# Kernel tuning notes

Measured on AMD Instinct MI355X. Metric: run time of the kernel, lower is better.

Reference implementation:

```python
import jax, jax.numpy as jnp
import numpy as np

B, L, DIM = 2, 4096, 512
HEADS, KS = 8, 33
HEAD_DIM = DIM // HEADS
SCALE = HEAD_DIM ** -0.5


def setup_inputs() -> dict:
    key = jax.random.key(0)
    ks = jax.random.split(key, 5)
    s = 0.02
    return {
        "x": jax.random.normal(ks[0], (B, L, DIM), dtype=jnp.float32),
        "w_qkv": jax.random.normal(ks[1], (3 * DIM, DIM), dtype=jnp.float32) * s,
        "b_qkv": jax.random.normal(ks[2], (3 * DIM,), dtype=jnp.float32) * s,
        "w_proj": jax.random.normal(ks[3], (DIM, DIM), dtype=jnp.float32) * s,
        "b_proj": jax.random.normal(ks[4], (DIM,), dtype=jnp.float32) * s,
    }


def _na1d(q, k, v):
    # q,k,v: [B, L, H, d]. Each query i attends to KS tokens whose window
    # start is clamp(i - KS//2, 0, L-KS) (NATTEN boundary-clamped neighborhood).
    starts = jnp.clip(jnp.arange(L) - KS // 2, 0, L - KS)          # [L]
    idx = starts[:, None] + jnp.arange(KS)[None, :]                # [L, KS]
    k_g = k[:, idx]                                                # [B, L, KS, H, d]
    v_g = v[:, idx]                                                # [B, L, KS, H, d]
    scores = jnp.einsum("blhd,blkhd->bhlk", q * SCALE, k_g)        # [B, H, L, KS]
    attn = jax.nn.softmax(scores, axis=-1)
    out = jnp.einsum("bhlk,blkhd->blhd", attn, v_g)                # [B, L, H, d]
    return out


def reference(x, w_qkv, b_qkv, w_proj, b_proj):
    qkv = x @ w_qkv.T + b_qkv                                      # [B, L, 3*DIM]
    qkv = qkv.reshape(B, L, 3, HEADS, HEAD_DIM)
    q, k, v = qkv[:, :, 0], qkv[:, :, 1], qkv[:, :, 2]
    out = _na1d(q, k, v).reshape(B, L, DIM)
    return out @ w_proj.T + b_proj
```

## Files before the change

kernel.cpp:

```cpp
#include <hip/hip_runtime.h>
#include <hip/hip_bf16.h>

#define B_ 2
#define L_ 4096
#define DIM_ 512
#define HEADS_ 8
#define HDIM_ 64
#define KS_ 33
#define QKS_ 1024

typedef __bf16 bf16;
typedef __bf16 bf16x4 __attribute__((ext_vector_type(4)));
typedef __bf16 bf16x8 __attribute__((ext_vector_type(8)));
typedef float f32x4 __attribute__((ext_vector_type(4)));

typedef __attribute__((address_space(3))) void lds_void;
typedef __attribute__((address_space(1))) const void glb_void;

__device__ __forceinline__ void async_cp16(const bf16* g, bf16* l)
{
    __builtin_amdgcn_global_load_lds((glb_void*)g, (lds_void*)l, 16, 0, 0);
}

__global__ __launch_bounds__(256)
void cvt_all(const float* __restrict__ x,  const float* __restrict__ wq,
             const float* __restrict__ bq, const float* __restrict__ wp,
             const float* __restrict__ bp,
             bf16* __restrict__ xb,  bf16* __restrict__ wqb,
             bf16* __restrict__ bqb, bf16* __restrict__ wpb,
             bf16* __restrict__ bpb)
{
    const int blk = blockIdx.x;
    const float* src; bf16* dst; int n, base;
    if (blk < 2048)       { src = x;  dst = xb;  n = 4194304; base = blk; }
    else if (blk < 2432)  { src = wq; dst = wqb; n = 786432;  base = blk - 2048; }
    else if (blk < 2560)  { src = wp; dst = wpb; n = 262144;  base = blk - 2432; }
    else if (blk == 2560) { src = bq; dst = bqb; n = 1536;    base = 0; }
    else                  { src = bp; dst = bpb; n = 512;     base = 0; }
    int i = base * 2048 + threadIdx.x * 8;
    if (i + 8 <= n) {
        float4 a = *(const float4*)(src + i);
        float4 b = *(const float4*)(src + i + 4);
        bf16x8 o;
        o[0] = (bf16)a.x; o[1] = (bf16)a.y; o[2] = (bf16)a.z; o[3] = (bf16)a.w;
        o[4] = (bf16)b.x; o[5] = (bf16)b.y; o[6] = (bf16)b.z; o[7] = (bf16)b.w;
        *(bf16x8*)(dst + i) = o;
    }
}

__global__ __launch_bounds__(256)
void gemm_qkv(const bf16* __restrict__ A, const bf16* __restrict__ W,
              const bf16* __restrict__ bias,
              bf16* __restrict__ qk, bf16* __restrict__ vT)
{
    __shared__ bf16 As[128][64];
    __shared__ bf16 Bs[64][64];

    const int tid  = threadIdx.x;
    const int wave = tid >> 6;
    const int lane = tid & 63;
    const int wm   = (wave >> 1) * 64;
    const int wn   = (wave & 1) * 32;
    const int l16  = lane & 15;
    const int quad = lane >> 4;

    const int row0 = blockIdx.x * 128;
    const int col0 = blockIdx.y * 64;
    const int K    = DIM_;

    f32x4 acc[4][2] = {};

    for (int k0 = 0; k0 < K; k0 += 64) {
        #pragma unroll
        for (int it = 0; it < 6; ++it) {
            int f = it * 256 + tid;
            if (f < 1024) {
                int r = f >> 3, pc = f & 7, lc = pc ^ (r & 7);
                async_cp16(&A[(size_t)(row0 + r) * K + k0 + lc * 8], &As[r][pc * 8]);
            } else {
                int g = f - 1024;
                int r = g >> 3, pc = g & 7, lc = pc ^ (r & 7);
                async_cp16(&W[(size_t)(col0 + r) * K + k0 + lc * 8], &Bs[r][pc * 8]);
            }
        }
        __syncthreads();

        #pragma unroll
        for (int ks = 0; ks < 2; ++ks) {
            bf16x8 af[4], bfr[2];
            #pragma unroll
            for (int i = 0; i < 4; ++i) {
                int ra = wm + i * 16 + l16;
                af[i] = *(const bf16x8*)(&As[ra][((ks * 4 + quad) ^ (ra & 7)) * 8]);
            }
            #pragma unroll
            for (int i = 0; i < 2; ++i) {
                int rb = wn + i * 16 + l16;
                bfr[i] = *(const bf16x8*)(&Bs[rb][((ks * 4 + quad) ^ (rb & 7)) * 8]);
            }
            #pragma unroll
            for (int mi = 0; mi < 4; ++mi)
                #pragma unroll
                for (int ni = 0; ni < 2; ++ni)
                    acc[mi][ni] = __builtin_amdgcn_mfma_f32_16x16x32_bf16(
                        af[mi], bfr[ni], acc[mi][ni], 0, 0, 0);
        }
        __syncthreads();
    }

    if (col0 < 1024) {
        #pragma unroll
        for (int ni = 0; ni < 2; ++ni) {
            int n = col0 + wn + ni * 16 + l16;
            float bv = (float)bias[n];
            #pragma unroll
            for (int mi = 0; mi < 4; ++mi) {
                int mrow = row0 + wm + mi * 16 + quad * 4;
                #pragma unroll
                for (int r = 0; r < 4; ++r)
                    qk[(size_t)(mrow + r) * QKS_ + n] = (bf16)(acc[mi][ni][r] + bv);
            }
        }
    } else {
        #pragma unroll
        for (int ni = 0; ni < 2; ++ni) {
            int nf = col0 + wn + ni * 16 + l16;
            float bv = (float)bias[nf];
            int hd = nf - 1024;
            #pragma unroll
            for (int mi = 0; mi < 4; ++mi) {
                int m = row0 + wm + mi * 16 + quad * 4;
                int b = m >> 12;
                int l = m & (L_ - 1);
                bf16x4 v4;
                #pragma unroll
                for (int r = 0; r < 4; ++r) v4[r] = (bf16)(acc[mi][ni][r] + bv);
                *(bf16x4*)(vT + ((size_t)(b * DIM_ + hd)) * L_ + l) = v4;
            }
        }
    }
}

__global__ __launch_bounds__(256)
void gemm_proj(const bf16* __restrict__ A, const bf16* __restrict__ W,
               const bf16* __restrict__ bias, float* __restrict__ C)
{
    __shared__ bf16 As[64][64];
    __shared__ bf16 Bs[64][64];

    const int tid  = threadIdx.x;
    const int wave = tid >> 6;
    const int lane = tid & 63;
    const int wm   = (wave & 1) * 32;
    const int wn   = (wave >> 1) * 32;
    const int l16  = lane & 15;
    const int quad = lane >> 4;

    const int row0 = blockIdx.x * 64;
    const int col0 = blockIdx.y * 64;
    const int K    = DIM_;

    f32x4 acc[2][2] = {};

    for (int k0 = 0; k0 < K; k0 += 64) {
        #pragma unroll
        for (int it = 0; it < 4; ++it) {
            int f = it * 256 + tid;
            if (f < 512) {
                int r = f >> 3, pc = f & 7, lc = pc ^ (r & 7);
                async_cp16(&A[(size_t)(row0 + r) * K + k0 + lc * 8], &As[r][pc * 8]);
            } else {
                int g = f - 512;
                int r = g >> 3, pc = g & 7, lc = pc ^ (r & 7);
                async_cp16(&W[(size_t)(col0 + r) * K + k0 + lc * 8], &Bs[r][pc * 8]);
            }
        }
        __syncthreads();

        #pragma unroll
        for (int ks = 0; ks < 2; ++ks) {
            bf16x8 af[2], bfr[2];
            #pragma unroll
            for (int i = 0; i < 2; ++i) {
                int ra = wm + i * 16 + l16;
                af[i] = *(const bf16x8*)(&As[ra][((ks * 4 + quad) ^ (ra & 7)) * 8]);
            }
            #pragma unroll
            for (int i = 0; i < 2; ++i) {
                int rb = wn + i * 16 + l16;
                bfr[i] = *(const bf16x8*)(&Bs[rb][((ks * 4 + quad) ^ (rb & 7)) * 8]);
            }
            #pragma unroll
            for (int mi = 0; mi < 2; ++mi)
                #pragma unroll
                for (int ni = 0; ni < 2; ++ni)
                    acc[mi][ni] = __builtin_amdgcn_mfma_f32_16x16x32_bf16(
                        af[mi], bfr[ni], acc[mi][ni], 0, 0, 0);
        }
        __syncthreads();
    }

    #pragma unroll
    for (int ni = 0; ni < 2; ++ni) {
        int n = col0 + wn + ni * 16 + l16;
        float bv = (float)bias[n];
        #pragma unroll
        for (int mi = 0; mi < 2; ++mi) {
            int mrow = row0 + wm + mi * 16 + quad * 4;
            #pragma unroll
            for (int r = 0; r < 4; ++r)
                C[(size_t)(mrow + r) * DIM_ + n] = acc[mi][ni][r] + bv;
        }
    }
}

__global__ __launch_bounds__(128)
void na1d_attn_mfma(const bf16* __restrict__ qk, const bf16* __restrict__ vT,
                    bf16* __restrict__ att)
{
    __shared__ bf16 Klds[64 * 64];
    __shared__ bf16 Plds[2][16][72];

    const int tid  = threadIdx.x;
    const int wave = tid >> 6;
    const int lane = tid & 63;
    const int l16  = lane & 15;
    const int quad = lane >> 4;

    const int xcd  = blockIdx.x & 7;
    const int s    = blockIdx.x >> 3;
    const int qtr  = s & 3;
    const int jj   = (s >> 2) & 3;
    const int h    = (s >> 4) & 7;
    const int b    = s >> 7;
    const int p    = jj * 8 + xcd;
    const int Q0   = p * 128 + qtr * 32;

    const size_t rowbase = (size_t)b * L_;

    #pragma unroll
    for (int i = 0; i < 4; ++i) {
        int ck = i * 128 + tid;
        int r  = ck >> 3;
        int pc = ck & 7;
        int lc = pc ^ (r & 7);
        int g  = Q0 - 16 + r;
        g = g < 0 ? 0 : (g > L_ - 1 ? L_ - 1 : g);
        async_cp16(qk + (rowbase + g) * QKS_ + DIM_ + h * HDIM_ + lc * 8,
                   Klds + (size_t)ck * 8);
    }

    const int q0w = Q0 + wave * 16;
    const bf16* qptr = qk + (rowbase + q0w + l16) * QKS_ + h * HDIM_ + quad * 8;
    bf16x8 qf0 = *(const bf16x8*)(qptr);
    bf16x8 qf1 = *(const bf16x8*)(qptr + 32);

    int k_base = q0w - 16;
    if (k_base > L_ - 48) k_base = L_ - 48;
    if (k_base < 0) k_base = 0;
    const int rel = k_base - (Q0 - 16);

    __syncthreads();

    f32x4 sacc[3] = {};
    #pragma unroll
    for (int t = 0; t < 3; ++t) {
        int r = rel + t * 16 + l16;
        bf16x8 kf0 = *(const bf16x8*)(Klds + r * 64 + ((quad ^ (r & 7)) * 8));
        bf16x8 kf1 = *(const bf16x8*)(Klds + r * 64 + (((4 + quad) ^ (r & 7)) * 8));
        sacc[t] = __builtin_amdgcn_mfma_f32_16x16x32_bf16(qf0, kf0, sacc[t], 0, 0, 0);
        sacc[t] = __builtin_amdgcn_mfma_f32_16x16x32_bf16(qf1, kf1, sacc[t], 0, 0, 0);
    }

    int offr[4];
    #pragma unroll
    for (int r = 0; r < 4; ++r) {
        int lq = q0w + quad * 4 + r;
        int st = lq - KS_ / 2;
        if (st < 0) st = 0;
        if (st > L_ - KS_) st = L_ - KS_;
        offr[r] = st - k_base;
    }
    float sv[3][4];
    #pragma unroll
    for (int t = 0; t < 3; ++t) {
        int j = t * 16 + l16;
        #pragma unroll
        for (int r = 0; r < 4; ++r) {
            float xv = sacc[t][r] * 0.125f;
            sv[t][r] = (j >= offr[r] && j <= offr[r] + 32) ? xv : -1e30f;
        }
    }

    float mr[4], sum[4];
    #pragma unroll
    for (int r = 0; r < 4; ++r)
        mr[r] = fmaxf(fmaxf(sv[0][r], sv[1][r]), sv[2][r]);
    #pragma unroll
    for (int o = 1; o < 16; o <<= 1)
        #pragma unroll
        for (int r = 0; r < 4; ++r)
            mr[r] = fmaxf(mr[r], __shfl_xor(mr[r], o, 64));
    #pragma unroll
    for (int t = 0; t < 3; ++t)
        #pragma unroll
        for (int r = 0; r < 4; ++r)
            sv[t][r] = __expf(sv[t][r] - mr[r]);
    #pragma unroll
    for (int r = 0; r < 4; ++r)
        sum[r] = sv[0][r] + sv[1][r] + sv[2][r];
    #pragma unroll
    for (int o = 1; o < 16; o <<= 1)
        #pragma unroll
        for (int r = 0; r < 4; ++r)
            sum[r] += __shfl_xor(sum[r], o, 64);
    #pragma unroll
    for (int r = 0; r < 4; ++r) {
        float inv = 1.0f / sum[r];
        #pragma unroll
        for (int t = 0; t < 3; ++t) sv[t][r] *= inv;
    }

    bf16* P = &Plds[wave][0][0];
    {
        int rr = lane >> 2;
        int c0 = 48 + (lane & 3) * 4;
        *(bf16x4*)(&P[rr * 72 + c0]) = (bf16x4){(bf16)0.f, (bf16)0.f, (bf16)0.f, (bf16)0.f};
    }
    #pragma unroll
    for (int t = 0; t < 3; ++t)
        #pragma unroll
        for (int r = 0; r < 4; ++r)
            P[(quad * 4 + r) * 72 + t * 16 + l16] = (bf16)sv[t][r];
    __syncthreads();

    bf16x8 pf0 = *(const bf16x8*)(&P[l16 * 72 + quad * 8]);
    bf16x8 pf1 = *(const bf16x8*)(&P[l16 * 72 + 32 + quad * 8]);

    const bf16* vbase = vT + (size_t)(b * DIM_ + h * HDIM_) * L_;
    int c1 = k_base + quad * 8;
    int c2 = k_base + 32 + quad * 8;
    if (c2 > L_ - 8) c2 = L_ - 8;
    f32x4 o[4] = {};
    #pragma unroll
    for (int t = 0; t < 4; ++t) {
        const bf16* vrow = vbase + (size_t)(t * 16 + l16) * L_;
        bf16x8 vf0 = *(const bf16x8*)(vrow + c1);
        bf16x8 vf1 = *(const bf16x8*)(vrow + c2);
        o[t] = __builtin_amdgcn_mfma_f32_16x16x32_bf16(pf0, vf0, o[t], 0, 0, 0);
        o[t] = __builtin_amdgcn_mfma_f32_16x16x32_bf16(pf1, vf1, o[t], 0, 0, 0);
    }

    bf16* orow = att + (rowbase + q0w) * DIM_ + h * HDIM_;
    #pragma unroll
    for (int t = 0; t < 4; ++t)
        #pragma unroll
        for (int r = 0; r < 4; ++r)
            orow[(size_t)(quad * 4 + r) * DIM_ + t * 16 + l16] = (bf16)o[t][r];
}

extern "C" void kernel_launch(void* const* d_in, const int* in_sizes, int n_in,
                              void* d_out, int out_size, void* d_ws, size_t ws_size,
                              hipStream_t stream) {
    const int n_x  = B_ * L_ * DIM_;
    const int n_wq = 3 * DIM_ * DIM_;
    const int n_bq = 3 * DIM_;
    const int n_wp = DIM_ * DIM_;
    const int n_bp = DIM_;

    char* ws = (char*)d_ws;
    bf16* xb  = (bf16*)ws;
    bf16* wqb = xb  + n_x;
    bf16* bqb = wqb + n_wq;
    bf16* wpb = bqb + n_bq;
    bf16* bpb = wpb + n_wp;
    bf16* qk  = bpb + n_bp;
    bf16* vT  = qk  + (size_t)8192 * 1024;
    bf16* att = vT  + (size_t)B_ * DIM_ * L_;

    float* out = (float*)d_out;
    const int M = B_ * L_;

    cvt_all<<<2562, 256, 0, stream>>>(
        (const float*)d_in[0], (const float*)d_in[1], (const float*)d_in[2],
        (const float*)d_in[3], (const float*)d_in[4],
        xb, wqb, bqb, wpb, bpb);

    gemm_qkv<<<dim3(M / 128, (3 * DIM_) / 64), 256, 0, stream>>>(
        xb, wqb, bqb, qk, vT);

    na1d_attn_mfma<<<dim3((B_ * HEADS_ * L_) / 32), 128, 0, stream>>>(qk, vT, att);

    gemm_proj<<<dim3(M / 64, DIM_ / 64), 256, 0, stream>>>(
        att, wpb, bpb, out);
}
```

Before: 118.5 us.

## Fuse x fp32-to-bf16 conversion into QKV GEMM, enlarge attention and proj tiles

Drops the separate conversion pass over x and instead converts fp32 x to bf16 while staging it into LDS inside the QKV GEMM, which removes a full write and reread of the bf16 copy of x. The attention kernel now handles 64 queries with 4 waves per block, sharing a 96-row K tile. The projection GEMM reuses the 128-row tile shape. The trade-off is that the x loads in the QKV GEMM become synchronous register loads instead of async LDS copies, and x is reloaded and reconverted for each of the 24 column blocks.

```diff
diff --git a/kernel.cpp b/kernel.cpp
--- a/kernel.cpp
+++ b/kernel.cpp
@@ -23,20 +23,17 @@
 }
 
 __global__ __launch_bounds__(256)
-void cvt_all(const float* __restrict__ x,  const float* __restrict__ wq,
-             const float* __restrict__ bq, const float* __restrict__ wp,
-             const float* __restrict__ bp,
-             bf16* __restrict__ xb,  bf16* __restrict__ wqb,
-             bf16* __restrict__ bqb, bf16* __restrict__ wpb,
-             bf16* __restrict__ bpb)
+void cvt_w(const float* __restrict__ wq, const float* __restrict__ bq,
+           const float* __restrict__ wp, const float* __restrict__ bp,
+           bf16* __restrict__ wqb, bf16* __restrict__ bqb,
+           bf16* __restrict__ wpb, bf16* __restrict__ bpb)
 {
     const int blk = blockIdx.x;
     const float* src; bf16* dst; int n, base;
-    if (blk < 2048)       { src = x;  dst = xb;  n = 4194304; base = blk; }
-    else if (blk < 2432)  { src = wq; dst = wqb; n = 786432;  base = blk - 2048; }
-    else if (blk < 2560)  { src = wp; dst = wpb; n = 262144;  base = blk - 2432; }
-    else if (blk == 2560) { src = bq; dst = bqb; n = 1536;    base = 0; }
-    else                  { src = bp; dst = bpb; n = 512;     base = 0; }
+    if (blk < 384)        { src = wq; dst = wqb; n = 786432; base = blk; }
+    else if (blk < 512)   { src = wp; dst = wpb; n = 262144; base = blk - 384; }
+    else if (blk == 512)  { src = bq; dst = bqb; n = 1536;   base = 0; }
+    else                  { src = bp; dst = bpb; n = 512;    base = 0; }
     int i = base * 2048 + threadIdx.x * 8;
     if (i + 8 <= n) {
         float4 a = *(const float4*)(src + i);
@@ -49,9 +46,107 @@
 }
 
 __global__ __launch_bounds__(256)
-void gemm_qkv(const bf16* __restrict__ A, const bf16* __restrict__ W,
+void gemm_qkv(const float* __restrict__ X, const bf16* __restrict__ W,
               const bf16* __restrict__ bias,
               bf16* __restrict__ qk, bf16* __restrict__ vT)
+{
+    __shared__ bf16 As[128][64];
+    __shared__ bf16 Bs[64][64];
+
+    const int tid  = threadIdx.x;
+    const int wave = tid >> 6;
+    const int lane = tid & 63;
+    const int wm   = (wave >> 1) * 64;
+    const int wn   = (wave & 1) * 32;
+    const int l16  = lane & 15;
+    const int quad = lane >> 4;
+
+    const int row0 = blockIdx.x * 128;
+    const int col0 = blockIdx.y * 64;
+    const int K    = DIM_;
+
+    f32x4 acc[4][2] = {};
+
+    for (int k0 = 0; k0 < K; k0 += 64) {
+        #pragma unroll
+        for (int it = 0; it < 2; ++it) {
+            int g = it * 256 + tid;
+            int r = g >> 3, pc = g & 7, lc = pc ^ (r & 7);
+            async_cp16(&W[(size_t)(col0 + r) * K + k0 + lc * 8], &Bs[r][pc * 8]);
+        }
+        #pragma unroll
+        for (int it = 0; it < 4; ++it) {
+            int f = it * 256 + tid;
+            int r = f >> 3, pc = f & 7, lc = pc ^ (r & 7);
+            const float* src = X + (size_t)(row0 + r) * K + k0 + lc * 8;
+            float4 a = *(const float4*)src;
+            float4 b = *(const float4*)(src + 4);
+            bf16x8 o;
+            o[0] = (bf16)a.x; o[1] = (bf16)a.y; o[2] = (bf16)a.z; o[3] = (bf16)a.w;
+            o[4] = (bf16)b.x; o[5] = (bf16)b.y; o[6] = (bf16)b.z; o[7] = (bf16)b.w;
+            *(bf16x8*)(&As[r][pc * 8]) = o;
+        }
+        __syncthreads();
+
+        #pragma unroll
+        for (int ks = 0; ks < 2; ++ks) {
+            bf16x8 af[4], bfr[2];
+            #pragma unroll
+            for (int i = 0; i < 4; ++i) {
+                int ra = wm + i * 16 + l16;
+                af[i] = *(const bf16x8*)(&As[ra][((ks * 4 + quad) ^ (ra & 7)) * 8]);
+            }
+            #pragma unroll
+            for (int i = 0; i < 2; ++i) {
+                int rb = wn + i * 16 + l16;
+                bfr[i] = *(const bf16x8*)(&Bs[rb][((ks * 4 + quad) ^ (rb & 7)) * 8]);
+            }
+            #pragma unroll
+            for (int mi = 0; mi < 4; ++mi)
+                #pragma unroll
+                for (int ni = 0; ni < 2; ++ni)
+                    acc[mi][ni] = __builtin_amdgcn_mfma_f32_16x16x32_bf16(
+                        af[mi], bfr[ni], acc[mi][ni], 0, 0, 0);
+        }
+        __syncthreads();
+    }
+
+    if (col0 < 1024) {
+        #pragma unroll
+        for (int ni = 0; ni < 2; ++ni) {
+            int n = col0 + wn + ni * 16 + l16;
+            float bv = (float)bias[n];
+            #pragma unroll
+            for (int mi = 0; mi < 4; ++mi) {
+                int mrow = row0 + wm + mi * 16 + quad * 4;
+                #pragma unroll
+                for (int r = 0; r < 4; ++r)
+                    qk[(size_t)(mrow + r) * QKS_ + n] = (bf16)(acc[mi][ni][r] + bv);
+            }
+        }
+    } else {
+        #pragma unroll
+        for (int ni = 0; ni < 2; ++ni) {
+            int nf = col0 + wn + ni * 16 + l16;
+            float bv = (float)bias[nf];
+            int hd = nf - 1024;
+            #pragma unroll
+            for (int mi = 0; mi < 4; ++mi) {
+                int m = row0 + wm + mi * 16 + quad * 4;
+                int b = m >> 12;
+                int l = m & (L_ - 1);
+                bf16x4 v4;
+                #pragma unroll
+                for (int r = 0; r < 4; ++r) v4[r] = (bf16)(acc[mi][ni][r] + bv);
+                *(bf16x4*)(vT + ((size_t)(b * DIM_ + hd)) * L_ + l) = v4;
+            }
+        }
+    }
+}
+
+__global__ __launch_bounds__(256)
+void gemm_proj(const bf16* __restrict__ A, const bf16* __restrict__ W,
+               const bf16* __restrict__ bias, float* __restrict__ C)
 {
     __shared__ bf16 As[128][64];
     __shared__ bf16 Bs[64][64];
@@ -108,104 +203,12 @@
         __syncthreads();
     }
 
-    if (col0 < 1024) {
-        #pragma unroll
-        for (int ni = 0; ni < 2; ++ni) {
-            int n = col0 + wn + ni * 16 + l16;
-            float bv = (float)bias[n];
-            #pragma unroll
-            for (int mi = 0; mi < 4; ++mi) {
-                int mrow = row0 + wm + mi * 16 + quad * 4;
-                #pragma unroll
-                for (int r = 0; r < 4; ++r)
-                    qk[(size_t)(mrow + r) * QKS_ + n] = (bf16)(acc[mi][ni][r] + bv);
-            }
-        }
-    } else {
-        #pragma unroll
-        for (int ni = 0; ni < 2; ++ni) {
-            int nf = col0 + wn + ni * 16 + l16;
-            float bv = (float)bias[nf];
-            int hd = nf - 1024;
-            #pragma unroll
-            for (int mi = 0; mi < 4; ++mi) {
-                int m = row0 + wm + mi * 16 + quad * 4;
-                int b = m >> 12;
-                int l = m & (L_ - 1);
-                bf16x4 v4;
-                #pragma unroll
-                for (int r = 0; r < 4; ++r) v4[r] = (bf16)(acc[mi][ni][r] + bv);
-                *(bf16x4*)(vT + ((size_t)(b * DIM_ + hd)) * L_ + l) = v4;
-            }
-        }
-    }
-}
-
-__global__ __launch_bounds__(256)
-void gemm_proj(const bf16* __restrict__ A, const bf16* __restrict__ W,
-               const bf16* __restrict__ bias, float* __restrict__ C)
-{
-    __shared__ bf16 As[64][64];
-    __shared__ bf16 Bs[64][64];
-
-    const int tid  = threadIdx.x;
-    const int wave = tid >> 6;
-    const int lane = tid & 63;
-    const int wm   = (wave & 1) * 32;
-    const int wn   = (wave >> 1) * 32;
-    const int l16  = lane & 15;
-    const int quad = lane >> 4;
-
-    const int row0 = blockIdx.x * 64;
-    const int col0 = blockIdx.y * 64;
-    const int K    = DIM_;
-
-    f32x4 acc[2][2] = {};
-
-    for (int k0 = 0; k0 < K; k0 += 64) {
-        #pragma unroll
-        for (int it = 0; it < 4; ++it) {
-            int f = it * 256 + tid;
-            if (f < 512) {
-                int r = f >> 3, pc = f & 7, lc = pc ^ (r & 7);
-                async_cp16(&A[(size_t)(row0 + r) * K + k0 + lc * 8], &As[r][pc * 8]);
-            } else {
-                int g = f - 512;
-                int r = g >> 3, pc = g & 7, lc = pc ^ (r & 7);
-                async_cp16(&W[(size_t)(col0 + r) * K + k0 + lc * 8], &Bs[r][pc * 8]);
-            }
-        }
-        __syncthreads();
-
-        #pragma unroll
-        for (int ks = 0; ks < 2; ++ks) {
-            bf16x8 af[2], bfr[2];
-            #pragma unroll
-            for (int i = 0; i < 2; ++i) {
-                int ra = wm + i * 16 + l16;
-                af[i] = *(const bf16x8*)(&As[ra][((ks * 4 + quad) ^ (ra & 7)) * 8]);
-            }
-            #pragma unroll
-            for (int i = 0; i < 2; ++i) {
-                int rb = wn + i * 16 + l16;
-                bfr[i] = *(const bf16x8*)(&Bs[rb][((ks * 4 + quad) ^ (rb & 7)) * 8]);
-            }
-            #pragma unroll
-            for (int mi = 0; mi < 2; ++mi)
-                #pragma unroll
-                for (int ni = 0; ni < 2; ++ni)
-                    acc[mi][ni] = __builtin_amdgcn_mfma_f32_16x16x32_bf16(
-                        af[mi], bfr[ni], acc[mi][ni], 0, 0, 0);
-        }
-        __syncthreads();
-    }
-
     #pragma unroll
     for (int ni = 0; ni < 2; ++ni) {
         int n = col0 + wn + ni * 16 + l16;
         float bv = (float)bias[n];
         #pragma unroll
-        for (int mi = 0; mi < 2; ++mi) {
+        for (int mi = 0; mi < 4; ++mi) {
             int mrow = row0 + wm + mi * 16 + quad * 4;
             #pragma unroll
             for (int r = 0; r < 4; ++r)
@@ -214,12 +217,12 @@
     }
 }
 
-__global__ __launch_bounds__(128)
+__global__ __launch_bounds__(256)
 void na1d_attn_mfma(const bf16* __restrict__ qk, const bf16* __restrict__ vT,
                     bf16* __restrict__ att)
 {
-    __shared__ bf16 Klds[64 * 64];
-    __shared__ bf16 Plds[2][16][72];
+    __shared__ bf16 Klds[96 * 64];
+    __shared__ bf16 Plds[4][16][72];
 
     const int tid  = threadIdx.x;
     const int wave = tid >> 6;
@@ -229,18 +232,18 @@
 
     const int xcd  = blockIdx.x & 7;
     const int s    = blockIdx.x >> 3;
-    const int qtr  = s & 3;
-    const int jj   = (s >> 2) & 3;
-    const int h    = (s >> 4) & 7;
-    const int b    = s >> 7;
+    const int jj   = s & 3;
+    const int half = (s >> 2) & 1;
+    const int h    = (s >> 3) & 7;
+    const int b    = s >> 6;
     const int p    = jj * 8 + xcd;
-    const int Q0   = p * 128 + qtr * 32;
+    const int Q0   = p * 128 + half * 64;
 
     const size_t rowbase = (size_t)b * L_;
 
     #pragma unroll
-    for (int i = 0; i < 4; ++i) {
-        int ck = i * 128 + tid;
+    for (int i = 0; i < 3; ++i) {
+        int ck = i * 256 + tid;
         int r  = ck >> 3;
         int pc = ck & 7;
         int lc = pc ^ (r & 7);
@@ -362,15 +365,13 @@
 extern "C" void kernel_launch(void* const* d_in, const int* in_sizes, int n_in,
                               void* d_out, int out_size, void* d_ws, size_t ws_size,
                               hipStream_t stream) {
-    const int n_x  = B_ * L_ * DIM_;
     const int n_wq = 3 * DIM_ * DIM_;
     const int n_bq = 3 * DIM_;
     const int n_wp = DIM_ * DIM_;
     const int n_bp = DIM_;
 
     char* ws = (char*)d_ws;
-    bf16* xb  = (bf16*)ws;
-    bf16* wqb = xb  + n_x;
+    bf16* wqb = (bf16*)ws;
     bf16* bqb = wqb + n_wq;
     bf16* wpb = bqb + n_bq;
     bf16* bpb = wpb + n_wp;
@@ -381,16 +382,16 @@
     float* out = (float*)d_out;
     const int M = B_ * L_;
 
-    cvt_all<<<2562, 256, 0, stream>>>(
-        (const float*)d_in[0], (const float*)d_in[1], (const float*)d_in[2],
+    cvt_w<<<514, 256, 0, stream>>>(
+        (const float*)d_in[1], (const float*)d_in[2],
         (const float*)d_in[3], (const float*)d_in[4],
-        xb, wqb, bqb, wpb, bpb);
+        wqb, bqb, wpb, bpb);
 
     gemm_qkv<<<dim3(M / 128, (3 * DIM_) / 64), 256, 0, stream>>>(
-        xb, wqb, bqb, qk, vT);
-
-    na1d_attn_mfma<<<dim3((B_ * HEADS_ * L_) / 32), 128, 0, stream>>>(qk, vT, att);
-
-    gemm_proj<<<dim3(M / 64, DIM_ / 64), 256, 0, stream>>>(
+        (const float*)d_in[0], wqb, bqb, qk, vT);
+
+    na1d_attn_mfma<<<dim3((B_ * HEADS_ * L_) / 64), 256, 0, stream>>>(qk, vT, att);
+
+    gemm_proj<<<dim3(M / 128, DIM_ / 64), 256, 0, stream>>>(
         att, wpb, bpb, out);
 }
```

After: 122.6 us. +3.5%, slower.
